# Optimization experiments

Measured on AMD Instinct MI355X. Metric: run time of the kernel, lower is better.

Reference implementation:

```python
import jax, jax.numpy as jnp
import numpy as np

KSIZE = 3  # median window

def median_blur(x, k):
    # x: [B, C, H, W]; zero padding (k-1)//2, median over k*k window
    # (matches kornia's conv2d-with-binary-kernels + median implementation)
    p = (k - 1) // 2
    xp = jnp.pad(x, ((0, 0), (0, 0), (p, p), (p, p)))
    B, C, H, W = x.shape
    # stack k*k shifted views -> [B, C, H, W, k*k] (k*k=9, small static loop)
    patches = jnp.stack(
        [xp[:, :, i:i + H, j:j + W] for i in range(k) for j in range(k)],
        axis=-1,
    )
    return jnp.median(patches, axis=-1)


def setup_inputs() -> dict:
    key = jax.random.key(0)
    k1, k2, k3 = jax.random.split(key, 3)
    B, C, H, W = 32, 256, 64, 64
    x = jax.random.normal(k1, (B, C, H, W), dtype=jnp.float32)
    # 1x1 conv weight [out_c, in_c] (the trailing 1x1 spatial dims are squeezed)
    conv_w = jax.random.normal(k2, (C, C), dtype=jnp.float32) * (1.0 / np.sqrt(C))
    conv_b = jax.random.normal(k3, (C,), dtype=jnp.float32) * 0.01
    return {"x": x, "conv_w": conv_w, "conv_b": conv_b}


def reference(x, conv_w, conv_b):
    x_denoised = median_blur(x, KSIZE)  # [B, C, H, W]
    # 1x1 conv == per-pixel channel mixing GEMM
    conv_out = jnp.einsum("oc,bchw->bohw", conv_w, x_denoised) + conv_b[None, :, None, None]
    return x + conv_out
```

## Files before the change

### kernel.cpp

```cpp
#include <hip/hip_runtime.h>

typedef float f32x4 __attribute__((ext_vector_type(4)));
typedef __bf16 bf16x8 __attribute__((ext_vector_type(8)));
typedef unsigned short u16x8 __attribute__((ext_vector_type(8)));

__device__ __forceinline__ unsigned short f2bf(float f) {
  union { float f; unsigned u; } v; v.f = f;
  unsigned r = v.u + 0x7FFFu + ((v.u >> 16) & 1u);
  return (unsigned short)(r >> 16);
}

__device__ __forceinline__ float min3f(float a, float b, float c) {
  return fminf(fminf(a, b), c);
}
__device__ __forceinline__ float max3f(float a, float b, float c) {
  return fmaxf(fmaxf(a, b), c);
}
__device__ __forceinline__ float med3f(float a, float b, float c) {
  return __builtin_amdgcn_fmed3f(a, b, c);
}

__device__ __forceinline__ void gload_lds16(const void* g, void* l) {
  __builtin_amdgcn_global_load_lds(
      (const __attribute__((address_space(1))) void*)g,
      (__attribute__((address_space(3))) void*)l, 16, 0, 0);
}

__global__ void wconv_k(const float* __restrict__ w, unsigned short* __restrict__ wbf) {
  int idx  = blockIdx.x * 256 + threadIdx.x;
  int lane = idx & 63;
  int ob   = (idx >> 6) & 15;
  int ks   = idx >> 10;
  int o = (ob << 4) + (lane & 15);
  int c = (ks << 5) + ((lane >> 4) << 3);
  const float* src = w + (o << 8) + c;
  f32x4 v0 = *(const f32x4*)src;
  f32x4 v1 = *(const f32x4*)(src + 4);
  u16x8 ov;
  ov[0] = f2bf(v0[0]); ov[1] = f2bf(v0[1]); ov[2] = f2bf(v0[2]); ov[3] = f2bf(v0[3]);
  ov[4] = f2bf(v1[0]); ov[5] = f2bf(v1[1]); ov[6] = f2bf(v1[2]); ov[7] = f2bf(v1[3]);
  *(u16x8*)(wbf + (idx << 3)) = ov;
}

__launch_bounds__(256, 3)
__global__ void fused_k(const float* __restrict__ x,
                        const unsigned short* __restrict__ wbf,
                        const float* __restrict__ bias,
                        float* __restrict__ out) {
  __shared__ float Xs[96][64];
  __shared__ unsigned short Bt[64][40];
  __shared__ float BiasS[256];

  const int t   = threadIdx.x;
  const int blk = blockIdx.x;
  const int swz = ((blk & 7) << 8) | (blk >> 3);
  const int b   = swz >> 6;
  const int r   = swz & 63;
  const int lane = t & 63;
  const int w    = t >> 6;
  const int g    = lane >> 4;
  const int l15  = lane & 15;

  const int ci  = t >> 3;
  const int s   = t & 7;
  const int px0 = s << 3;
  const int cw  = ci ^ ((s & 3) << 3);
  const bool rT = (r >= 1), rB = (r <= 62);
  const bool hasL = (s > 0), hasR = (s < 7);

  BiasS[t] = bias[t];

  const float* xb = x + ((size_t)b << 20);

  unsigned soff[6];
  #pragma unroll
  for (int p = 0; p < 6; ++p) {
    int row = w * 24 + (p << 2) + (lane >> 4);
    int cip = (row * 171) >> 9;
    int drp = row - cip * 3;
    int gr  = r + drp - 1;
    gr = gr < 0 ? 0 : (gr > 63 ? 63 : gr);
    int bG  = (lane & 15) ^ (cip & 7);
    soff[p] = ((unsigned)cip << 14) + ((unsigned)gr << 8) + ((unsigned)bG << 4);
  }

  #pragma unroll
  for (int p = 0; p < 6; ++p)
    gload_lds16((const char*)xb + soff[p], &Xs[w * 24 + (p << 2)][0]);

  f32x4 acc[4][4];
  #pragma unroll
  for (int m = 0; m < 4; ++m)
    #pragma unroll
    for (int n = 0; n < 4; ++n)
      acc[m][n] = (f32x4){0.f, 0.f, 0.f, 0.f};

  const int ri0 = ci * 3;
  const int sig = ci & 7;
  const int bAi = ((s << 1)) ^ sig;
  const int bBi = ((s << 1) | 1) ^ sig;
  const int bLi = (((s << 1) - 1) & 15) ^ sig;
  const int bRi = (((s << 1) + 2) & 15) ^ sig;

  __syncthreads();

  #pragma unroll
  for (int ks = 0; ks < 8; ++ks) {
    bf16x8 a[4];
    #pragma unroll
    for (int m = 0; m < 4; ++m) {
      const int fidx = (((ks << 4) + (w << 2) + m) << 6) + lane;
      a[m] = __builtin_bit_cast(bf16x8, *(const u16x8*)(wbf + ((size_t)fidx << 3)));
    }

    float R[3][10];
    #pragma unroll
    for (int dr = 0; dr < 3; ++dr) {
      const float* rp = &Xs[ri0 + dr][0];
      f32x4 va = *(const f32x4*)(rp + (bAi << 2));
      f32x4 vb = *(const f32x4*)(rp + (bBi << 2));
      R[dr][0] = hasL ? rp[(bLi << 2) + 3] : 0.f;
      R[dr][9] = hasR ? rp[(bRi << 2)]     : 0.f;
      #pragma unroll
      for (int j = 0; j < 4; ++j) { R[dr][1 + j] = va[j]; R[dr][5 + j] = vb[j]; }
    }
    if (!rT) {
      #pragma unroll
      for (int j = 0; j < 10; ++j) R[0][j] = 0.f;
    }
    if (!rB) {
      #pragma unroll
      for (int j = 0; j < 10; ++j) R[2][j] = 0.f;
    }

    float mn[10], md[10], mx[10];
    #pragma unroll
    for (int j = 0; j < 10; ++j) {
      mn[j] = min3f(R[0][j], R[1][j], R[2][j]);
      md[j] = med3f(R[0][j], R[1][j], R[2][j]);
      mx[j] = max3f(R[0][j], R[1][j], R[2][j]);
    }
    #pragma unroll
    for (int i = 0; i < 8; ++i) {
      float t0 = max3f(mn[i], mn[i+1], mn[i+2]);
      float t1 = med3f(md[i], md[i+1], md[i+2]);
      float t2 = min3f(mx[i], mx[i+1], mx[i+2]);
      Bt[px0 + i][cw] = f2bf(med3f(t0, t1, t2));
    }

    __syncthreads();

    if (ks < 7) {
      const unsigned kso = (unsigned)(ks + 1) << 19;
      #pragma unroll
      for (int p = 0; p < 6; ++p)
        gload_lds16((const char*)xb + (soff[p] + kso), &Xs[w * 24 + (p << 2)][0]);
    }

    bf16x8 bb[4];
    #pragma unroll
    for (int n = 0; n < 4; ++n) {
      const int px = (n << 4) + l15;
      const int gc = (g ^ ((px >> 3) & 3)) << 3;
      bb[n] = __builtin_bit_cast(bf16x8, *(const u16x8*)&Bt[px][gc]);
    }
    #pragma unroll
    for (int m = 0; m < 4; ++m)
      #pragma unroll
      for (int n = 0; n < 4; ++n)
        acc[m][n] = __builtin_amdgcn_mfma_f32_16x16x32_bf16(a[m], bb[n], acc[m][n], 0, 0, 0);

    if (ks < 7) __syncthreads();
  }

  #pragma unroll
  for (int m = 0; m < 4; ++m) {
    const int o = (w << 6) + (m << 4) + (g << 2);
    #pragma unroll
    for (int n = 0; n < 4; ++n) {
      const int px = (n << 4) + l15;
      const size_t base = ((((size_t)b << 8) + (size_t)o) << 12) + ((size_t)r << 6) + (size_t)px;
      #pragma unroll
      for (int q = 0; q < 4; ++q) {
        const size_t idx = base + ((size_t)q << 12);
        out[idx] = x[idx] + acc[m][n][q] + BiasS[o + q];
      }
    }
  }
}

extern "C" void kernel_launch(void* const* d_in, const int* in_sizes, int n_in,
                              void* d_out, int out_size, void* d_ws, size_t ws_size,
                              hipStream_t stream) {
  const float* x  = (const float*)d_in[0];
  const float* cw = (const float*)d_in[1];
  const float* cb = (const float*)d_in[2];
  float* out = (float*)d_out;
  unsigned short* wbf = (unsigned short*)d_ws;

  hipLaunchKernelGGL(wconv_k, dim3(32), dim3(256), 0, stream, cw, wbf);
  hipLaunchKernelGGL(fused_k, dim3(2048), dim3(256), 0, stream, x, wbf, cb, out);
}
```

Baseline: 74.09 us.

## Double-buffer LDS tiles and swap MFMA operands for vectorized epilogue

Double-buffers the staged input and the median tile in LDS. The next channel chunk's global loads and median computation now overlap the current chunk's MFMAs, which cuts the barriers per step from two to one. The MFMA operands are swapped so each lane holds four consecutive pixels, which lets the epilogue read x and write out as float4 instead of scalar accesses. Neighbor edge values come from lane shuffles rather than extra LDS reads, and s_setprio is raised around the MFMAs. LDS use roughly doubles, so launch bounds drop from 3 to 2 blocks per CU and occupancy falls.

```diff
diff --git a/kernel.cpp b/kernel.cpp
--- a/kernel.cpp
+++ b/kernel.cpp
@@ -42,14 +42,13 @@
   *(u16x8*)(wbf + (idx << 3)) = ov;
 }
 
-__launch_bounds__(256, 3)
+__launch_bounds__(256, 2)
 __global__ void fused_k(const float* __restrict__ x,
                         const unsigned short* __restrict__ wbf,
                         const float* __restrict__ bias,
                         float* __restrict__ out) {
-  __shared__ float Xs[96][64];
-  __shared__ unsigned short Bt[64][40];
-  __shared__ float BiasS[256];
+  __shared__ float Xs[2][96][64];
+  __shared__ unsigned short Bt[2][64][40];
 
   const int t   = threadIdx.x;
   const int blk = blockIdx.x;
@@ -68,9 +67,11 @@
   const bool rT = (r >= 1), rB = (r <= 62);
   const bool hasL = (s > 0), hasR = (s < 7);
 
-  BiasS[t] = bias[t];
-
   const float* xb = x + ((size_t)b << 20);
+
+  float bn[4];
+  #pragma unroll
+  for (int n = 0; n < 4; ++n) bn[n] = bias[(w << 6) + (n << 4) + l15];
 
   unsigned soff[6];
   #pragma unroll
@@ -84,45 +85,35 @@
     soff[p] = ((unsigned)cip << 14) + ((unsigned)gr << 8) + ((unsigned)bG << 4);
   }
 
-  #pragma unroll
-  for (int p = 0; p < 6; ++p)
-    gload_lds16((const char*)xb + soff[p], &Xs[w * 24 + (p << 2)][0]);
-
-  f32x4 acc[4][4];
-  #pragma unroll
-  for (int m = 0; m < 4; ++m)
-    #pragma unroll
-    for (int n = 0; n < 4; ++n)
-      acc[m][n] = (f32x4){0.f, 0.f, 0.f, 0.f};
-
   const int ri0 = ci * 3;
   const int sig = ci & 7;
   const int bAi = ((s << 1)) ^ sig;
   const int bBi = ((s << 1) | 1) ^ sig;
-  const int bLi = (((s << 1) - 1) & 15) ^ sig;
-  const int bRi = (((s << 1) + 2) & 15) ^ sig;
-
-  __syncthreads();
-
-  #pragma unroll
-  for (int ks = 0; ks < 8; ++ks) {
-    bf16x8 a[4];
-    #pragma unroll
-    for (int m = 0; m < 4; ++m) {
-      const int fidx = (((ks << 4) + (w << 2) + m) << 6) + lane;
-      a[m] = __builtin_bit_cast(bf16x8, *(const u16x8*)(wbf + ((size_t)fidx << 3)));
-    }
-
+
+  auto stage = [&](int step, int buf) {
+    const unsigned kso = (unsigned)step << 19;
+    #pragma unroll
+    for (int p = 0; p < 6; ++p)
+      gload_lds16((const char*)xb + (soff[p] + kso), &Xs[buf][w * 24 + (p << 2)][0]);
+  };
+
+  auto median_store = [&](int bufx, int bufb) {
+    f32x4 va[3], vb[3];
+    #pragma unroll
+    for (int dr = 0; dr < 3; ++dr) {
+      const float* rp = &Xs[bufx][ri0 + dr][0];
+      va[dr] = *(const f32x4*)(rp + (bAi << 2));
+      vb[dr] = *(const f32x4*)(rp + (bBi << 2));
+    }
     float R[3][10];
     #pragma unroll
     for (int dr = 0; dr < 3; ++dr) {
-      const float* rp = &Xs[ri0 + dr][0];
-      f32x4 va = *(const f32x4*)(rp + (bAi << 2));
-      f32x4 vb = *(const f32x4*)(rp + (bBi << 2));
-      R[dr][0] = hasL ? rp[(bLi << 2) + 3] : 0.f;
-      R[dr][9] = hasR ? rp[(bRi << 2)]     : 0.f;
-      #pragma unroll
-      for (int j = 0; j < 4; ++j) { R[dr][1 + j] = va[j]; R[dr][5 + j] = vb[j]; }
+      float le = __shfl_up(vb[dr][3], 1);
+      float re = __shfl_down(va[dr][0], 1);
+      R[dr][0] = hasL ? le : 0.f;
+      R[dr][9] = hasR ? re : 0.f;
+      #pragma unroll
+      for (int j = 0; j < 4; ++j) { R[dr][1 + j] = va[dr][j]; R[dr][5 + j] = vb[dr][j]; }
     }
     if (!rT) {
       #pragma unroll
@@ -132,7 +123,6 @@
       #pragma unroll
       for (int j = 0; j < 10; ++j) R[2][j] = 0.f;
     }
-
     float mn[10], md[10], mx[10];
     #pragma unroll
     for (int j = 0; j < 10; ++j) {
@@ -145,46 +135,67 @@
       float t0 = max3f(mn[i], mn[i+1], mn[i+2]);
       float t1 = med3f(md[i], md[i+1], md[i+2]);
       float t2 = min3f(mx[i], mx[i+1], mx[i+2]);
-      Bt[px0 + i][cw] = f2bf(med3f(t0, t1, t2));
-    }
-
-    __syncthreads();
-
-    if (ks < 7) {
-      const unsigned kso = (unsigned)(ks + 1) << 19;
-      #pragma unroll
-      for (int p = 0; p < 6; ++p)
-        gload_lds16((const char*)xb + (soff[p] + kso), &Xs[w * 24 + (p << 2)][0]);
-    }
-
-    bf16x8 bb[4];
+      Bt[bufb][px0 + i][cw] = f2bf(med3f(t0, t1, t2));
+    }
+  };
+
+  f32x4 acc[4][4];
+  #pragma unroll
+  for (int m = 0; m < 4; ++m)
+    #pragma unroll
+    for (int n = 0; n < 4; ++n)
+      acc[m][n] = (f32x4){0.f, 0.f, 0.f, 0.f};
+
+  stage(0, 0);
+  stage(1, 1);
+  __syncthreads();
+  median_store(0, 0);
+  __syncthreads();
+
+  #pragma unroll
+  for (int ks = 0; ks < 8; ++ks) {
+    if (ks < 6) stage(ks + 2, ks & 1);
+
+    bf16x8 wf[4];
     #pragma unroll
     for (int n = 0; n < 4; ++n) {
-      const int px = (n << 4) + l15;
+      const int fidx = (((ks << 4) + (w << 2) + n) << 6) + lane;
+      wf[n] = __builtin_bit_cast(bf16x8, *(const u16x8*)(wbf + ((size_t)fidx << 3)));
+    }
+
+    if (ks < 7) median_store((ks + 1) & 1, (ks + 1) & 1);
+
+    bf16x8 pa[4];
+    #pragma unroll
+    for (int m = 0; m < 4; ++m) {
+      const int px = (m << 4) + l15;
       const int gc = (g ^ ((px >> 3) & 3)) << 3;
-      bb[n] = __builtin_bit_cast(bf16x8, *(const u16x8*)&Bt[px][gc]);
-    }
+      pa[m] = __builtin_bit_cast(bf16x8, *(const u16x8*)&Bt[ks & 1][px][gc]);
+    }
+
+    __builtin_amdgcn_s_setprio(1);
     #pragma unroll
     for (int m = 0; m < 4; ++m)
       #pragma unroll
       for (int n = 0; n < 4; ++n)
-        acc[m][n] = __builtin_amdgcn_mfma_f32_16x16x32_bf16(a[m], bb[n], acc[m][n], 0, 0, 0);
+        acc[m][n] = __builtin_amdgcn_mfma_f32_16x16x32_bf16(pa[m], wf[n], acc[m][n], 0, 0, 0);
+    __builtin_amdgcn_s_setprio(0);
 
     if (ks < 7) __syncthreads();
   }
 
   #pragma unroll
   for (int m = 0; m < 4; ++m) {
-    const int o = (w << 6) + (m << 4) + (g << 2);
     #pragma unroll
     for (int n = 0; n < 4; ++n) {
-      const int px = (n << 4) + l15;
-      const size_t base = ((((size_t)b << 8) + (size_t)o) << 12) + ((size_t)r << 6) + (size_t)px;
-      #pragma unroll
-      for (int q = 0; q < 4; ++q) {
-        const size_t idx = base + ((size_t)q << 12);
-        out[idx] = x[idx] + acc[m][n][q] + BiasS[o + q];
-      }
+      const int o = (w << 6) + (n << 4) + l15;
+      const size_t idx = ((((size_t)b << 8) + (size_t)o) << 12) + ((size_t)r << 6)
+                       + (size_t)((m << 4) + (g << 2));
+      f32x4 xv = *(const f32x4*)(x + idx);
+      f32x4 res;
+      #pragma unroll
+      for (int q = 0; q < 4; ++q) res[q] = xv[q] + acc[m][n][q] + bn[n];
+      *(f32x4*)(out + idx) = res;
     }
   }
 }
```

New measurement: 91.08 us. 22.9% more time.
